# Kernel tuning notes

Hardware: AMD Instinct MI355X
Metric: run time of the kernel (lower is better)

Reference implementation:

```python
import jax, jax.numpy as jnp
import numpy as np

N_NODES = 100_000
N_RAND_EDGES = 1_600_000
NEG_SLOPE = 0.2


def setup_inputs() -> dict:
    key = jax.random.key(0)
    ks = jax.random.split(key, 12)
    inputs = jax.random.normal(ks[0], (N_NODES, 128), dtype=jnp.float32)
    # params (fc weight [in, H*D], attn vectors [H, D]); 0.1 scale for stability
    W0 = jax.random.normal(ks[1], (128, 4 * 32), dtype=jnp.float32) * 0.1
    al0 = jax.random.normal(ks[2], (4, 32), dtype=jnp.float32) * 0.1
    ar0 = jax.random.normal(ks[3], (4, 32), dtype=jnp.float32) * 0.1
    W1 = jax.random.normal(ks[4], (4 * 32, 4 * 32), dtype=jnp.float32) * 0.1
    al1 = jax.random.normal(ks[5], (4, 32), dtype=jnp.float32) * 0.1
    ar1 = jax.random.normal(ks[6], (4, 32), dtype=jnp.float32) * 0.1
    W2 = jax.random.normal(ks[7], (4 * 32, 1 * 40), dtype=jnp.float32) * 0.1
    al2 = jax.random.normal(ks[8], (1, 40), dtype=jnp.float32) * 0.1
    ar2 = jax.random.normal(ks[9], (1, 40), dtype=jnp.float32) * 0.1
    # edge list: random edges + self loops (guarantees in-degree >= 1)
    src = jnp.concatenate([
        jax.random.randint(ks[10], (N_RAND_EDGES,), 0, N_NODES, dtype=jnp.int32),
        jnp.arange(N_NODES, dtype=jnp.int32)])
    dst = jnp.concatenate([
        jax.random.randint(ks[11], (N_RAND_EDGES,), 0, N_NODES, dtype=jnp.int32),
        jnp.arange(N_NODES, dtype=jnp.int32)])
    return dict(inputs=inputs, W0=W0, al0=al0, ar0=ar0, W1=W1, al1=al1,
                ar1=ar1, W2=W2, al2=al2, ar2=ar2, src=src, dst=dst, empty=0)


def _gat_conv(h, W, al, ar, src, dst):
    """DGL-style GATConv (no dropout, no residual, no bias). Returns [N, H, D]."""
    N = h.shape[0]
    H, D = al.shape
    feat = (h @ W).reshape(N, H, D)
    el = jnp.sum(feat * al, axis=-1)  # [N, H]
    er = jnp.sum(feat * ar, axis=-1)  # [N, H]
    e = jax.nn.leaky_relu(el[src] + er[dst], negative_slope=NEG_SLOPE)  # [E, H]
    # edge softmax over incoming edges of each destination node (stable)
    m = jax.ops.segment_max(e, dst, num_segments=N)          # [N, H]
    ee = jnp.exp(e - m[dst])                                 # [E, H]
    denom = jax.ops.segment_sum(ee, dst, num_segments=N)     # [N, H]
    alpha = ee / denom[dst]                                  # [E, H]
    # gather source features, weight by attention, scatter-sum to destinations
    out = jax.ops.segment_sum(feat[src] * alpha[:, :, None], dst, num_segments=N)
    return out


def reference(inputs, W0, al0, ar0, W1, al1, ar1, W2, al2, ar2, src, dst, empty):
    N = inputs.shape[0]
    h = inputs
    for (W, al, ar) in ((W0, al0, ar0), (W1, al1, ar1)):
        h = jax.nn.elu(_gat_conv(h, W, al, ar, src, dst)).reshape(N, -1)
    logits = _gat_conv(h, W2, al2, ar2, src, dst).mean(axis=1)  # [N, num_classes]
    return jax.nn.log_softmax(logits, axis=1)
```

## Files before the change

kernel.cpp:

```cpp
#include <hip/hip_runtime.h>
#include <math.h>

typedef unsigned int uint32;
typedef unsigned short ushort;
typedef __attribute__((ext_vector_type(8))) short short8;
typedef __attribute__((ext_vector_type(4))) float f32x4;

__device__ inline uint32 bf16rn(float x){
  uint32 b = __float_as_uint(x);
  return (b + 0x7fffu + ((b>>16)&1u)) >> 16;
}
__device__ inline float bf16lo(uint32 v){ return __uint_as_float(v<<16); }
__device__ inline float bf16hi(uint32 v){ return __uint_as_float(v & 0xffff0000u); }

#define BKT_SHIFT 9
#define BKTCAP 12288
#define PCHUNK 4096
#define FB40S 64

__global__ __launch_bounds__(256) void k_partition(const int* __restrict__ src, const int* __restrict__ dst,
                        int* __restrict__ bkt_cursor, uint32* __restrict__ pairs, int E){
  __shared__ int cnt[512];
  __shared__ int base[512];
  int t = threadIdx.x;
  int blockBase = blockIdx.x * PCHUNK;
  for (int i=t; i<512; i+=256) cnt[i]=0;
  __syncthreads();
  #pragma unroll
  for (int i=0; i<PCHUNK/1024; i++){
    int e0 = blockBase + (i*256 + t)*4;
    if (e0+3 < E){
      int4 d4 = *(const int4*)&dst[e0];
      atomicAdd(&cnt[d4.x>>BKT_SHIFT],1);
      atomicAdd(&cnt[d4.y>>BKT_SHIFT],1);
      atomicAdd(&cnt[d4.z>>BKT_SHIFT],1);
      atomicAdd(&cnt[d4.w>>BKT_SHIFT],1);
    } else {
      for (int e=e0; e<E && e<e0+4; e++) atomicAdd(&cnt[dst[e]>>BKT_SHIFT],1);
    }
  }
  __syncthreads();
  for (int i=t; i<512; i+=256){
    int c = cnt[i];
    base[i] = c ? atomicAdd(&bkt_cursor[i], c) : 0;
    cnt[i] = 0;
  }
  __syncthreads();
  #pragma unroll
  for (int i=0; i<PCHUNK/1024; i++){
    int e0 = blockBase + (i*256 + t)*4;
    if (e0+3 < E){
      int4 s4 = *(const int4*)&src[e0];
      int4 d4 = *(const int4*)&dst[e0];
      int bx, pos;
      bx=d4.x>>BKT_SHIFT; pos=base[bx]+atomicAdd(&cnt[bx],1); if(pos<BKTCAP) pairs[(size_t)bx*BKTCAP+pos]=(uint32)s4.x|((uint32)(d4.x&511)<<22);
      bx=d4.y>>BKT_SHIFT; pos=base[bx]+atomicAdd(&cnt[bx],1); if(pos<BKTCAP) pairs[(size_t)bx*BKTCAP+pos]=(uint32)s4.y|((uint32)(d4.y&511)<<22);
      bx=d4.z>>BKT_SHIFT; pos=base[bx]+atomicAdd(&cnt[bx],1); if(pos<BKTCAP) pairs[(size_t)bx*BKTCAP+pos]=(uint32)s4.z|((uint32)(d4.z&511)<<22);
      bx=d4.w>>BKT_SHIFT; pos=base[bx]+atomicAdd(&cnt[bx],1); if(pos<BKTCAP) pairs[(size_t)bx*BKTCAP+pos]=(uint32)s4.w|((uint32)(d4.w&511)<<22);
    } else {
      for (int e=e0; e<E && e<e0+4; e++){
        int s=src[e], d=dst[e];
        int bx=d>>BKT_SHIFT; int pos=base[bx]+atomicAdd(&cnt[bx],1);
        if(pos<BKTCAP) pairs[(size_t)bx*BKTCAP+pos]=(uint32)s|((uint32)(d&511)<<22);
      }
    }
  }
}

__global__ __launch_bounds__(1024) void k_build(const int* __restrict__ bkt_cursor, int nb,
                        const uint32* __restrict__ pairs,
                        int* __restrict__ row_ptr, int* __restrict__ csr_src, int N){
  __shared__ int bscan[256];
  __shared__ int hist[512];
  __shared__ int sc[512];
  __shared__ int cur[512];
  int b = blockIdx.x;
  int t = threadIdx.x;
  int v0 = (t<256 && t<nb) ? min(bkt_cursor[t], BKTCAP) : 0;
  if (t<256) bscan[t] = v0;
  __syncthreads();
  int x0 = v0;
  for (int off=1; off<256; off<<=1){
    int y = (t<256 && t>=off) ? bscan[t-off] : 0;
    __syncthreads();
    if (t<256){ x0 += y; bscan[t] = x0; }
    __syncthreads();
  }
  int base = (b==0) ? 0 : bscan[b-1];
  if (b==0 && t==0) row_ptr[N] = bscan[nb-1];
  int cnt = bkt_cursor[b]; if (cnt > BKTCAP) cnt = BKTCAP;
  const uint32* p = pairs + (size_t)b*BKTCAP;
  if (t<512) hist[t]=0;
  __syncthreads();
  for (int i=t; i<cnt; i+=1024) atomicAdd(&hist[p[i]>>22], 1);
  __syncthreads();
  int v = (t<512)? hist[t] : 0;
  if (t<512) sc[t]=v;
  __syncthreads();
  int x=v;
  for (int off=1; off<512; off<<=1){
    int y = (t<512 && t>=off)? sc[t-off] : 0;
    __syncthreads();
    if (t<512){ x+=y; sc[t]=x; }
    __syncthreads();
  }
  if (t<512){
    int excl = x - v;
    int gnode = (b<<BKT_SHIFT) + t;
    if (gnode < N) row_ptr[gnode] = base + excl;
    cur[t] = excl;
  }
  __syncthreads();
  for (int i=t; i<cnt; i+=1024){
    uint32 e = p[i];
    int pos = atomicAdd(&cur[e>>22], 1);
    csr_src[base + pos] = (int)(e & 0x3FFFFFu);
  }
}

template<bool BF16A>
__global__ __launch_bounds__(256) void k_gemm128_mfma(const void* __restrict__ Av, const float* __restrict__ W,
                        const float* __restrict__ al, const float* __restrict__ ar,
                        ushort* __restrict__ Fb, float* __restrict__ el, float* __restrict__ er, int N){
  __shared__ __align__(16) ushort Wlds[128*128];
  __shared__ __align__(16) ushort Alds[64*128];
  __shared__ float sal[128], sar[128];
  int t = threadIdx.x;
  int rowBase = blockIdx.x*64;
  for (int i=t; i<8192; i+=256){
    int col = i & 127;
    int k2  = (i >> 7) * 2;
    float w0 = W[(size_t)k2*128 + col];
    float w1 = W[(size_t)(k2+1)*128 + col];
    uint32 pk = bf16rn(w0) | (bf16rn(w1)<<16);
    int byte = col*256 + k2*2;
    byte ^= (col&7)<<4;
    *(uint32*)((char*)Wlds + byte) = pk;
  }
  if (t < 128){ sal[t] = al[t]; sar[t] = ar[t]; }
  {
    int row = t>>2, k0 = (t&3)*32;
    int grow = rowBase + row;
    uint32 pk[16];
    if (grow < N){
      if constexpr (BF16A){
        const ushort* Ab = (const ushort*)Av;
        const uint4* ap = (const uint4*)(Ab + (size_t)grow*128 + k0);
        #pragma unroll
        for (int q=0;q<4;q++){ uint4 u = ap[q]; pk[q*4]=u.x; pk[q*4+1]=u.y; pk[q*4+2]=u.z; pk[q*4+3]=u.w; }
      } else {
        const float* Af = (const float*)Av;
        #pragma unroll
        for (int j=0;j<16;j++){
          float2 v = *(const float2*)(Af + (size_t)grow*128 + k0 + j*2);
          pk[j] = bf16rn(v.x) | (bf16rn(v.y)<<16);
        }
      }
    } else {
      #pragma unroll
      for (int j=0;j<16;j++) pk[j]=0u;
    }
    #pragma unroll
    for (int q=0;q<4;q++){
      int byte = row*256 + (k0 + q*8)*2;
      byte ^= (row&7)<<4;
      *(uint4*)((char*)Alds + byte) = make_uint4(pk[q*4],pk[q*4+1],pk[q*4+2],pk[q*4+3]);
    }
  }
  __syncthreads();
  int wid = t>>6, lane = t&63;
  int strip = wid*16;
  int lrow = lane & 15;
  int lk   = (lane>>4)*8;
  int swz  = (lrow&7)<<4;
  f32x4 acc[8];
  #pragma unroll
  for (int tc=0; tc<8; tc++) acc[tc] = (f32x4){0.f,0.f,0.f,0.f};
  #pragma unroll
  for (int kstep=0; kstep<4; kstep++){
    int kb = (kstep*32 + lk)*2;
    short8 bfrag = *(const short8*)((const char*)Alds + (((strip+lrow)*256 + kb) ^ swz));
    #pragma unroll
    for (int tc=0; tc<8; tc++){
      short8 afrag = *(const short8*)((const char*)Wlds + (((tc*16+lrow)*256 + kb) ^ swz));
      acc[tc] = __builtin_amdgcn_mfma_f32_16x16x32_bf16(afrag, bfrag, acc[tc], 0, 0, 0);
    }
  }
  int row = rowBase + strip + lrow;
  int cq = (lane>>4)*4;
  #pragma unroll
  for (int tc=0; tc<8; tc++){
    if (row < N){
      uint32 u0 = bf16rn(acc[tc][0]) | (bf16rn(acc[tc][1])<<16);
      uint32 u1 = bf16rn(acc[tc][2]) | (bf16rn(acc[tc][3])<<16);
      *(uint2*)(Fb + (size_t)row*128 + tc*16 + cq) = make_uint2(u0,u1);
    }
  }
  float hl[4] = {0.f,0.f,0.f,0.f};
  float hr[4] = {0.f,0.f,0.f,0.f};
  #pragma unroll
  for (int tc=0; tc<8; tc++){
    int cbase = tc*16 + cq;
    int h = tc>>1;
    #pragma unroll
    for (int r=0;r<4;r++){
      hl[h] = fmaf(acc[tc][r], sal[cbase+r], hl[h]);
      hr[h] = fmaf(acc[tc][r], sar[cbase+r], hr[h]);
    }
  }
  #pragma unroll
  for (int h=0;h<4;h++){
    hl[h] += __shfl_xor(hl[h],16); hl[h] += __shfl_xor(hl[h],32);
    hr[h] += __shfl_xor(hr[h],16); hr[h] += __shfl_xor(hr[h],32);
  }
  if (lane < 16 && row < N){
    *(float4*)&el[(size_t)row*4] = make_float4(hl[0],hl[1],hl[2],hl[3]);
    *(float4*)&er[(size_t)row*4] = make_float4(hr[0],hr[1],hr[2],hr[3]);
  }
}

__global__ __launch_bounds__(256) void k_agg128(const uint32* __restrict__ Fu, const float* __restrict__ el,
                         const float* __restrict__ er, const int* __restrict__ row_ptr,
                         const int* __restrict__ csr_src, ushort* __restrict__ out, int N){
  __shared__ float wlds[4][272];
  int t = threadIdx.x;
  int lane = t & 63;
  int wv = t >> 6;
  int node = (blockIdx.x*blockDim.x + t)>>6;
  if (__builtin_amdgcn_readfirstlane(node) >= N) return;
  int h = lane>>4;
  int i0 = lane & 15;
  float erv = er[(size_t)node*4+h];
  int beg = row_ptr[node], end = row_ptr[node+1];
  int ubeg = __builtin_amdgcn_readfirstlane(beg);
  int uend = __builtin_amdgcn_readfirstlane(end);
  int udeg = uend - ubeg;
  int sv = (lane < udeg) ? csr_src[ubeg+lane] : 0;
  int sn[4]; float evv[4];
  #pragma unroll
  for (int j=0;j<4;j++) sn[j] = __shfl(sv, i0 + 16*j);
  #pragma unroll
  for (int j=0;j<4;j++) evv[j] = el[(size_t)sn[j]*4+h];
  float w4[4];
  #pragma unroll
  for (int j=0;j<4;j++){
    float ev = evv[j] + erv;
    ev = ev>0.f ? ev : 0.2f*ev;
    w4[j] = (i0 + 16*j < udeg) ? __expf(ev) : 0.f;
  }
  float dsum = (w4[0]+w4[1]) + (w4[2]+w4[3]);
  dsum += __shfl_xor(dsum, 1);
  dsum += __shfl_xor(dsum, 2);
  dsum += __shfl_xor(dsum, 4);
  dsum += __shfl_xor(dsum, 8);
  int wb = h*68 + i0;
  wlds[wv][wb   ] = w4[0];
  wlds[wv][wb+16] = w4[1];
  wlds[wv][wb+32] = w4[2];
  wlds[wv][wb+48] = w4[3];
  const int* sp = csr_src + ubeg;
  const float* wp = &wlds[wv][h*68];
  float acc0=0.f, acc1=0.f;
  int nm = udeg > 64 ? 64 : udeg;
  uint32 vb[8];
  #pragma unroll
  for (int k=0;k<8;k++) vb[k] = (k<nm) ? Fu[(size_t)sp[k]*64 + lane] : 0u;
  int i=0;
  for (; i+16<=nm; i+=8){
    uint32 vn[8];
    #pragma unroll
    for (int k=0;k<8;k++) vn[k] = Fu[(size_t)sp[i+8+k]*64 + lane];
    #pragma unroll
    for (int k=0;k<8;k++){
      float wi = wp[i+k];
      acc0 = fmaf(wi, bf16lo(vb[k]), acc0);
      acc1 = fmaf(wi, bf16hi(vb[k]), acc1);
    }
    #pragma unroll
    for (int k=0;k<8;k++) vb[k]=vn[k];
  }
  {
    int lim = nm - i; if (lim > 8) lim = 8;
    #pragma unroll
    for (int k=0;k<8;k++) if (k<lim){
      float wi = wp[i+k];
      acc0 = fmaf(wi, bf16lo(vb[k]), acc0);
      acc1 = fmaf(wi, bf16hi(vb[k]), acc1);
    }
    for (int e=i+8; e<nm; e++){
      float wi = wp[e];
      uint32 v = Fu[(size_t)sp[e]*64 + lane];
      acc0 = fmaf(wi, bf16lo(v), acc0);
      acc1 = fmaf(wi, bf16hi(v), acc1);
    }
  }
  if (udeg > 64){
    for (int e=64; e<udeg; e++){
      int s = sp[e];
      float x = el[(size_t)s*4+h] + erv;
      x = x>0.f?x:0.2f*x; x=__expf(x);
      uint32 v = Fu[(size_t)s*64+lane];
      dsum += x;
      acc0 = fmaf(x, bf16lo(v), acc0);
      acc1 = fmaf(x, bf16hi(v), acc1);
    }
  }
  float inv = 1.0f/dsum;
  float o0 = acc0*inv, o1 = acc1*inv;
  o0 = o0>0.f ? o0 : expm1f(o0);
  o1 = o1>0.f ? o1 : expm1f(o1);
  uint32 uo = bf16rn(o0) | (bf16rn(o1)<<16);
  *(uint32*)(out + (size_t)node*128 + lane*2) = uo;
}

__global__ __launch_bounds__(256) void k_gemm42(const ushort* __restrict__ A, const float* __restrict__ W,
                        const float* __restrict__ al, const float* __restrict__ ar,
                        ushort* __restrict__ Fb, float* __restrict__ el, float* __restrict__ er, int N){
  __shared__ float wfull[128*48];
  __shared__ float hs[32][132];
  int t = threadIdx.x;
  int rowBase = blockIdx.x*128;
  for (int i=t; i<1280; i+=256){
    float4 v = *(const float4*)&W[i*4];
    int g = i*4;
    *(float4*)&wfull[(g/40)*48 + (g%40)] = v;
  }
  {
    int k = t & 127;
    const float* wrow = W + k*40;
    const float* a = (t < 128) ? al : ar;
    float s = 0.f;
    #pragma unroll
    for (int c=0;c<40;c++) s += wrow[c]*a[c];
    if (t < 128){
      wfull[k*48+40] = s;
      wfull[k*48+42] = 0.f; wfull[k*48+43] = 0.f; wfull[k*48+44] = 0.f;
    } else {
      wfull[k*48+41] = s;
      wfull[k*48+45] = 0.f; wfull[k*48+46] = 0.f; wfull[k*48+47] = 0.f;
    }
  }
  int c0 = (t&7)*6;
  int r0 = (t>>3)*4;
  float acc[4][6] = {};
  for (int kc=0; kc<128; kc+=32){
    {
      int row = t>>1; int kk0 = (t&1)*16;
      int grow = rowBase + row;
      if (grow < N){
        uint4 u0 = *(const uint4*)&A[(size_t)grow*128 + kc + kk0];
        uint4 u1 = *(const uint4*)&A[(size_t)grow*128 + kc + kk0 + 8];
        hs[kk0+ 0][row]=bf16lo(u0.x); hs[kk0+ 1][row]=bf16hi(u0.x);
        hs[kk0+ 2][row]=bf16lo(u0.y); hs[kk0+ 3][row]=bf16hi(u0.y);
        hs[kk0+ 4][row]=bf16lo(u0.z); hs[kk0+ 5][row]=bf16hi(u0.z);
        hs[kk0+ 6][row]=bf16lo(u0.w); hs[kk0+ 7][row]=bf16hi(u0.w);
        hs[kk0+ 8][row]=bf16lo(u1.x); hs[kk0+ 9][row]=bf16hi(u1.x);
        hs[kk0+10][row]=bf16lo(u1.y); hs[kk0+11][row]=bf16hi(u1.y);
        hs[kk0+12][row]=bf16lo(u1.z); hs[kk0+13][row]=bf16hi(u1.z);
        hs[kk0+14][row]=bf16lo(u1.w); hs[kk0+15][row]=bf16hi(u1.w);
      } else {
        #pragma unroll
        for (int j=0;j<16;j++) hs[kk0+j][row]=0.f;
      }
    }
    __syncthreads();
    #pragma unroll
    for (int k=0;k<32;k++){
      float4 av = *(const float4*)&hs[k][r0];
      const float* wp = &wfull[(kc+k)*48 + c0];
      float2 b01 = *(const float2*)&wp[0];
      float2 b23 = *(const float2*)&wp[2];
      float2 b45 = *(const float2*)&wp[4];
      float a4[4] = {av.x,av.y,av.z,av.w};
      float b6[6] = {b01.x,b01.y,b23.x,b23.y,b45.x,b45.y};
      #pragma unroll
      for (int r=0;r<4;r++)
        #pragma unroll
        for (int c=0;c<6;c++)
          acc[r][c] = fmaf(a4[r], b6[c], acc[r][c]);
    }
    __syncthreads();
  }
  #pragma unroll
  for (int r=0;r<4;r++){
    int row = rowBase + r0 + r;
    if (row >= N) break;
    if (c0 < 40){
      #pragma unroll
      for (int j=0;j<6;j+=2){
        int col = c0 + j;
        if (col < 40){
          uint32 u = bf16rn(acc[r][j]) | (bf16rn(acc[r][j+1])<<16);
          *(uint32*)(Fb + (size_t)row*FB40S + col) = u;
        }
      }
      if (c0 == 36){ el[row] = acc[r][4]; er[row] = acc[r][5]; }
    }
  }
}

__global__ __launch_bounds__(256) void k_agg40(const ushort* __restrict__ Fb, const float* __restrict__ el,
                       const float* __restrict__ er, const int* __restrict__ row_ptr,
                       const int* __restrict__ csr_src, float* __restrict__ out, int N){
  __shared__ float wlds[4][64];
  int t = threadIdx.x;
  int lane = t & 63;
  int wv = t >> 6;
  int node = (blockIdx.x*blockDim.x + t)>>6;
  if (__builtin_amdgcn_readfirstlane(node) >= N) return;
  bool act = lane<40;
  int l40 = act ? lane : 0;
  float erv = er[node];
  int beg = row_ptr[node], end = row_ptr[node+1];
  int ubeg = __builtin_amdgcn_readfirstlane(beg);
  int uend = __builtin_amdgcn_readfirstlane(end);
  int udeg = uend - ubeg;
  int sv = (lane < udeg) ? csr_src[ubeg+lane] : 0;
  float w = 0.f;
  if (lane < udeg){
    float ev = el[sv] + erv;
    ev = ev>0.f ? ev : 0.2f*ev;
    w = __expf(ev);
  }
  float dsum = w;
  dsum += __shfl_xor(dsum, 1);
  dsum += __shfl_xor(dsum, 2);
  dsum += __shfl_xor(dsum, 4);
  dsum += __shfl_xor(dsum, 8);
  dsum += __shfl_xor(dsum, 16);
  dsum += __shfl_xor(dsum, 32);
  wlds[wv][lane] = w;
  const int* sp = csr_src + ubeg;
  float acc=0.f;
  int nm = udeg > 64 ? 64 : udeg;
  ushort fb8[8];
  #pragma unroll
  for (int k=0;k<8;k++) fb8[k] = (k<nm) ? Fb[(size_t)sp[k]*FB40S + l40] : (ushort)0;
  int i=0;
  for (; i+16<=nm; i+=8){
    ushort fn[8];
    #pragma unroll
    for (int k=0;k<8;k++) fn[k] = Fb[(size_t)sp[i+8+k]*FB40S + l40];
    #pragma unroll
    for (int k=0;k<8;k++){
      float wi = wlds[wv][i+k];
      acc = fmaf(wi, __uint_as_float(((uint32)fb8[k])<<16), acc);
    }
    #pragma unroll
    for (int k=0;k<8;k++) fb8[k]=fn[k];
  }
  {
    int lim = nm - i; if (lim > 8) lim = 8;
    #pragma unroll
    for (int k=0;k<8;k++) if (k<lim){
      float wi = wlds[wv][i+k];
      acc = fmaf(wi, __uint_as_float(((uint32)fb8[k])<<16), acc);
    }
    for (int e=i+8; e<nm; e++){
      float wi = wlds[wv][e];
      ushort f = Fb[(size_t)sp[e]*FB40S + l40];
      acc = fmaf(wi, __uint_as_float(((uint32)f)<<16), acc);
    }
  }
  if (udeg > 64){
    for (int e=64; e<udeg; e++){
      int s = sp[e];
      float x = el[s] + erv;
      x = x>0.f?x:0.2f*x; x=__expf(x);
      ushort f = Fb[(size_t)s*FB40S + l40];
      dsum += x;
      acc = fmaf(x, __uint_as_float(((uint32)f)<<16), acc);
    }
  }
  float logit = acc/dsum;
  float m = act ? logit : -INFINITY;
  for (int off=32; off; off>>=1) m = fmaxf(m, __shfl_xor(m, off));
  float ex = act ? expf(logit - m) : 0.f;
  float ssum = ex;
  for (int off=32; off; off>>=1) ssum += __shfl_xor(ssum, off);
  if (act) out[(size_t)node*40 + lane] = logit - m - logf(ssum);
}

extern "C" void kernel_launch(void* const* d_in, const int* in_sizes, int n_in,
                              void* d_out, int out_size, void* d_ws, size_t ws_size,
                              hipStream_t stream){
  const float* inputs = (const float*)d_in[0];
  const float* W0  = (const float*)d_in[1];
  const float* al0 = (const float*)d_in[2];
  const float* ar0 = (const float*)d_in[3];
  const float* W1  = (const float*)d_in[4];
  const float* al1 = (const float*)d_in[5];
  const float* ar1 = (const float*)d_in[6];
  const float* W2  = (const float*)d_in[7];
  const float* al2 = (const float*)d_in[8];
  const float* ar2 = (const float*)d_in[9];
  const int* src = (const int*)d_in[10];
  const int* dst = (const int*)d_in[11];
  int N = in_sizes[0]/128;
  int E = in_sizes[10];
  int NB = (N + (1<<BKT_SHIFT) - 1) >> BKT_SHIFT;

  char* p = (char*)d_ws;
  auto carve = [&](size_t bytes)->char*{ char* q=p; p += ((bytes+255)/256)*256; return q; };
  ushort* Fb   = (ushort*)carve((size_t)N*128*2);
  ushort* Fb40 = (ushort*)carve((size_t)N*FB40S*2);
  ushort* bufH = (ushort*)carve((size_t)N*128*2);
  float* el  = (float*)carve((size_t)N*4*4);
  float* er  = (float*)carve((size_t)N*4*4);
  float* el2 = (float*)carve((size_t)N*4);
  float* er2 = (float*)carve((size_t)N*4);
  int* bkt_cursor  = (int*)carve((size_t)NB*4);
  int* row_ptr = (int*)carve((size_t)(N+1)*4);
  int* csr_src = (int*)carve((size_t)E*4);

  uint32* pairs = (uint32*)bufH;

  hipMemsetAsync(bkt_cursor, 0, (size_t)NB*4, stream);
  int nPB = (E + PCHUNK - 1) / PCHUNK;
  k_partition<<<nPB, 256, 0, stream>>>(src, dst, bkt_cursor, pairs, E);
  k_build    <<<NB, 1024, 0, stream>>>(bkt_cursor, NB, pairs, row_ptr, csr_src, N);

  int gRows = (N+63)/64;
  int gWave = (N+3)/4;
  int gRows42 = (N+127)/128;
  k_gemm128_mfma<false><<<gRows,256,0,stream>>>(inputs, W0, al0, ar0, Fb, el, er, N);
  k_agg128 <<<gWave,256,0,stream>>>((const uint32*)Fb, el, er, row_ptr, csr_src, bufH, N);
  k_gemm128_mfma<true><<<gRows,256,0,stream>>>(bufH, W1, al1, ar1, Fb, el, er, N);
  k_agg128 <<<gWave,256,0,stream>>>((const uint32*)Fb, el, er, row_ptr, csr_src, bufH, N);
  k_gemm42 <<<gRows42,256,0,stream>>>(bufH, W2, al2, ar2, Fb40, el2, er2, N);
  k_agg40  <<<gWave,256,0,stream>>>(Fb40, el2, er2, row_ptr, csr_src, (float*)d_out, N);
}
```

Baseline: 347.7 us.

## Merge edge partition and first-layer GEMM into one heterogeneous launch

```diff
diff --git a/kernel.cpp b/kernel.cpp
--- a/kernel.cpp
+++ b/kernel.cpp
@@ -18,52 +18,144 @@
 #define PCHUNK 4096
 #define FB40S 64
 
-__global__ __launch_bounds__(256) void k_partition(const int* __restrict__ src, const int* __restrict__ dst,
-                        int* __restrict__ bkt_cursor, uint32* __restrict__ pairs, int E){
-  __shared__ int cnt[512];
-  __shared__ int base[512];
+__global__ __launch_bounds__(256) void k_part_gemm0(const int* __restrict__ src, const int* __restrict__ dst,
+                        int* __restrict__ bkt_cursor, uint32* __restrict__ pairs, int E, int nPB,
+                        const float* __restrict__ A, const float* __restrict__ W,
+                        const float* __restrict__ al, const float* __restrict__ ar,
+                        ushort* __restrict__ Fb, float* __restrict__ el, float* __restrict__ er, int N){
+  __shared__ __align__(16) ushort Wlds[128*128];
+  __shared__ __align__(16) ushort Alds[64*128];
+  __shared__ float sal[128], sar[128];
   int t = threadIdx.x;
-  int blockBase = blockIdx.x * PCHUNK;
-  for (int i=t; i<512; i+=256) cnt[i]=0;
+  if (blockIdx.x < nPB){
+    int* cnt  = (int*)Wlds;
+    int* base = ((int*)Wlds) + 512;
+    int blockBase = blockIdx.x * PCHUNK;
+    for (int i=t; i<512; i+=256) cnt[i]=0;
+    __syncthreads();
+    #pragma unroll
+    for (int i=0; i<PCHUNK/1024; i++){
+      int e0 = blockBase + (i*256 + t)*4;
+      if (e0+3 < E){
+        int4 d4 = *(const int4*)&dst[e0];
+        atomicAdd(&cnt[d4.x>>BKT_SHIFT],1);
+        atomicAdd(&cnt[d4.y>>BKT_SHIFT],1);
+        atomicAdd(&cnt[d4.z>>BKT_SHIFT],1);
+        atomicAdd(&cnt[d4.w>>BKT_SHIFT],1);
+      } else {
+        for (int e=e0; e<E && e<e0+4; e++) atomicAdd(&cnt[dst[e]>>BKT_SHIFT],1);
+      }
+    }
+    __syncthreads();
+    for (int i=t; i<512; i+=256){
+      int c = cnt[i];
+      base[i] = c ? atomicAdd(&bkt_cursor[i], c) : 0;
+      cnt[i] = 0;
+    }
+    __syncthreads();
+    #pragma unroll
+    for (int i=0; i<PCHUNK/1024; i++){
+      int e0 = blockBase + (i*256 + t)*4;
+      if (e0+3 < E){
+        int4 s4 = *(const int4*)&src[e0];
+        int4 d4 = *(const int4*)&dst[e0];
+        int bx, pos;
+        bx=d4.x>>BKT_SHIFT; pos=base[bx]+atomicAdd(&cnt[bx],1); if(pos<BKTCAP) pairs[(size_t)bx*BKTCAP+pos]=(uint32)s4.x|((uint32)(d4.x&511)<<22);
+        bx=d4.y>>BKT_SHIFT; pos=base[bx]+atomicAdd(&cnt[bx],1); if(pos<BKTCAP) pairs[(size_t)bx*BKTCAP+pos]=(uint32)s4.y|((uint32)(d4.y&511)<<22);
+        bx=d4.z>>BKT_SHIFT; pos=base[bx]+atomicAdd(&cnt[bx],1); if(pos<BKTCAP) pairs[(size_t)bx*BKTCAP+pos]=(uint32)s4.z|((uint32)(d4.z&511)<<22);
+        bx=d4.w>>BKT_SHIFT; pos=base[bx]+atomicAdd(&cnt[bx],1); if(pos<BKTCAP) pairs[(size_t)bx*BKTCAP+pos]=(uint32)s4.w|((uint32)(d4.w&511)<<22);
+      } else {
+        for (int e=e0; e<E && e<e0+4; e++){
+          int s=src[e], d=dst[e];
+          int bx=d>>BKT_SHIFT; int pos=base[bx]+atomicAdd(&cnt[bx],1);
+          if(pos<BKTCAP) pairs[(size_t)bx*BKTCAP+pos]=(uint32)s|((uint32)(d&511)<<22);
+        }
+      }
+    }
+    return;
+  }
+  int rowBase = (blockIdx.x - nPB)*64;
+  for (int i=t; i<8192; i+=256){
+    int col = i & 127;
+    int k2  = (i >> 7) * 2;
+    float w0 = W[(size_t)k2*128 + col];
+    float w1 = W[(size_t)(k2+1)*128 + col];
+    uint32 pk = bf16rn(w0) | (bf16rn(w1)<<16);
+    int byte = col*256 + k2*2;
+    byte ^= (col&7)<<4;
+    *(uint32*)((char*)Wlds + byte) = pk;
+  }
+  if (t < 128){ sal[t] = al[t]; sar[t] = ar[t]; }
+  {
+    int row = t>>2, k0 = (t&3)*32;
+    int grow = rowBase + row;
+    uint32 pk[16];
+    if (grow < N){
+      #pragma unroll
+      for (int j=0;j<16;j++){
+        float2 v = *(const float2*)(A + (size_t)grow*128 + k0 + j*2);
+        pk[j] = bf16rn(v.x) | (bf16rn(v.y)<<16);
+      }
+    } else {
+      #pragma unroll
+      for (int j=0;j<16;j++) pk[j]=0u;
+    }
+    #pragma unroll
+    for (int q=0;q<4;q++){
+      int byte = row*256 + (k0 + q*8)*2;
+      byte ^= (row&7)<<4;
+      *(uint4*)((char*)Alds + byte) = make_uint4(pk[q*4],pk[q*4+1],pk[q*4+2],pk[q*4+3]);
+    }
+  }
   __syncthreads();
-  #pragma unroll
-  for (int i=0; i<PCHUNK/1024; i++){
-    int e0 = blockBase + (i*256 + t)*4;
-    if (e0+3 < E){
-      int4 d4 = *(const int4*)&dst[e0];
-      atomicAdd(&cnt[d4.x>>BKT_SHIFT],1);
-      atomicAdd(&cnt[d4.y>>BKT_SHIFT],1);
-      atomicAdd(&cnt[d4.z>>BKT_SHIFT],1);
-      atomicAdd(&cnt[d4.w>>BKT_SHIFT],1);
-    } else {
-      for (int e=e0; e<E && e<e0+4; e++) atomicAdd(&cnt[dst[e]>>BKT_SHIFT],1);
-    }
-  }
-  __syncthreads();
-  for (int i=t; i<512; i+=256){
-    int c = cnt[i];
-    base[i] = c ? atomicAdd(&bkt_cursor[i], c) : 0;
-    cnt[i] = 0;
-  }
-  __syncthreads();
-  #pragma unroll
-  for (int i=0; i<PCHUNK/1024; i++){
-    int e0 = blockBase + (i*256 + t)*4;
-    if (e0+3 < E){
-      int4 s4 = *(const int4*)&src[e0];
-      int4 d4 = *(const int4*)&dst[e0];
-      int bx, pos;
-      bx=d4.x>>BKT_SHIFT; pos=base[bx]+atomicAdd(&cnt[bx],1); if(pos<BKTCAP) pairs[(size_t)bx*BKTCAP+pos]=(uint32)s4.x|((uint32)(d4.x&511)<<22);
-      bx=d4.y>>BKT_SHIFT; pos=base[bx]+atomicAdd(&cnt[bx],1); if(pos<BKTCAP) pairs[(size_t)bx*BKTCAP+pos]=(uint32)s4.y|((uint32)(d4.y&511)<<22);
-      bx=d4.z>>BKT_SHIFT; pos=base[bx]+atomicAdd(&cnt[bx],1); if(pos<BKTCAP) pairs[(size_t)bx*BKTCAP+pos]=(uint32)s4.z|((uint32)(d4.z&511)<<22);
-      bx=d4.w>>BKT_SHIFT; pos=base[bx]+atomicAdd(&cnt[bx],1); if(pos<BKTCAP) pairs[(size_t)bx*BKTCAP+pos]=(uint32)s4.w|((uint32)(d4.w&511)<<22);
-    } else {
-      for (int e=e0; e<E && e<e0+4; e++){
-        int s=src[e], d=dst[e];
-        int bx=d>>BKT_SHIFT; int pos=base[bx]+atomicAdd(&cnt[bx],1);
-        if(pos<BKTCAP) pairs[(size_t)bx*BKTCAP+pos]=(uint32)s|((uint32)(d&511)<<22);
-      }
-    }
+  int wid = t>>6, lane = t&63;
+  int strip = wid*16;
+  int lrow = lane & 15;
+  int lk   = (lane>>4)*8;
+  int swz  = (lrow&7)<<4;
+  f32x4 acc[8];
+  #pragma unroll
+  for (int tc=0; tc<8; tc++) acc[tc] = (f32x4){0.f,0.f,0.f,0.f};
+  #pragma unroll
+  for (int kstep=0; kstep<4; kstep++){
+    int kb = (kstep*32 + lk)*2;
+    short8 bfrag = *(const short8*)((const char*)Alds + (((strip+lrow)*256 + kb) ^ swz));
+    #pragma unroll
+    for (int tc=0; tc<8; tc++){
+      short8 afrag = *(const short8*)((const char*)Wlds + (((tc*16+lrow)*256 + kb) ^ swz));
+      acc[tc] = __builtin_amdgcn_mfma_f32_16x16x32_bf16(afrag, bfrag, acc[tc], 0, 0, 0);
+    }
+  }
+  int row = rowBase + strip + lrow;
+  int cq = (lane>>4)*4;
+  #pragma unroll
+  for (int tc=0; tc<8; tc++){
+    if (row < N){
+      uint32 u0 = bf16rn(acc[tc][0]) | (bf16rn(acc[tc][1])<<16);
+      uint32 u1 = bf16rn(acc[tc][2]) | (bf16rn(acc[tc][3])<<16);
+      *(uint2*)(Fb + (size_t)row*128 + tc*16 + cq) = make_uint2(u0,u1);
+    }
+  }
+  float hl[4] = {0.f,0.f,0.f,0.f};
+  float hr[4] = {0.f,0.f,0.f,0.f};
+  #pragma unroll
+  for (int tc=0; tc<8; tc++){
+    int cbase = tc*16 + cq;
+    int h = tc>>1;
+    #pragma unroll
+    for (int r=0;r<4;r++){
+      hl[h] = fmaf(acc[tc][r], sal[cbase+r], hl[h]);
+      hr[h] = fmaf(acc[tc][r], sar[cbase+r], hr[h]);
+    }
+  }
+  #pragma unroll
+  for (int h=0;h<4;h++){
+    hl[h] += __shfl_xor(hl[h],16); hl[h] += __shfl_xor(hl[h],32);
+    hr[h] += __shfl_xor(hr[h],16); hr[h] += __shfl_xor(hr[h],32);
+  }
+  if (lane < 16 && row < N){
+    *(float4*)&el[(size_t)row*4] = make_float4(hl[0],hl[1],hl[2],hl[3]);
+    *(float4*)&er[(size_t)row*4] = make_float4(hr[0],hr[1],hr[2],hr[3]);
   }
 }
 
@@ -118,8 +210,7 @@
   }
 }
 
-template<bool BF16A>
-__global__ __launch_bounds__(256) void k_gemm128_mfma(const void* __restrict__ Av, const float* __restrict__ W,
+__global__ __launch_bounds__(256) void k_gemm128_mfma(const ushort* __restrict__ Ab, const float* __restrict__ W,
                         const float* __restrict__ al, const float* __restrict__ ar,
                         ushort* __restrict__ Fb, float* __restrict__ el, float* __restrict__ er, int N){
   __shared__ __align__(16) ushort Wlds[128*128];
@@ -143,19 +234,9 @@
     int grow = rowBase + row;
     uint32 pk[16];
     if (grow < N){
-      if constexpr (BF16A){
-        const ushort* Ab = (const ushort*)Av;
-        const uint4* ap = (const uint4*)(Ab + (size_t)grow*128 + k0);
-        #pragma unroll
-        for (int q=0;q<4;q++){ uint4 u = ap[q]; pk[q*4]=u.x; pk[q*4+1]=u.y; pk[q*4+2]=u.z; pk[q*4+3]=u.w; }
-      } else {
-        const float* Af = (const float*)Av;
-        #pragma unroll
-        for (int j=0;j<16;j++){
-          float2 v = *(const float2*)(Af + (size_t)grow*128 + k0 + j*2);
-          pk[j] = bf16rn(v.x) | (bf16rn(v.y)<<16);
-        }
-      }
+      const uint4* ap = (const uint4*)(Ab + (size_t)grow*128 + k0);
+      #pragma unroll
+      for (int q=0;q<4;q++){ uint4 u = ap[q]; pk[q*4]=u.x; pk[q*4+1]=u.y; pk[q*4+2]=u.z; pk[q*4+3]=u.w; }
     } else {
       #pragma unroll
       for (int j=0;j<16;j++) pk[j]=0u;
@@ -517,15 +598,15 @@
 
   hipMemsetAsync(bkt_cursor, 0, (size_t)NB*4, stream);
   int nPB = (E + PCHUNK - 1) / PCHUNK;
-  k_partition<<<nPB, 256, 0, stream>>>(src, dst, bkt_cursor, pairs, E);
-  k_build    <<<NB, 1024, 0, stream>>>(bkt_cursor, NB, pairs, row_ptr, csr_src, N);
-
   int gRows = (N+63)/64;
   int gWave = (N+3)/4;
   int gRows42 = (N+127)/128;
-  k_gemm128_mfma<false><<<gRows,256,0,stream>>>(inputs, W0, al0, ar0, Fb, el, er, N);
+
+  k_part_gemm0<<<nPB+gRows, 256, 0, stream>>>(src, dst, bkt_cursor, pairs, E, nPB,
+                                              inputs, W0, al0, ar0, Fb, el, er, N);
+  k_build <<<NB, 1024, 0, stream>>>(bkt_cursor, NB, pairs, row_ptr, csr_src, N);
   k_agg128 <<<gWave,256,0,stream>>>((const uint32*)Fb, el, er, row_ptr, csr_src, bufH, N);
-  k_gemm128_mfma<true><<<gRows,256,0,stream>>>(bufH, W1, al1, ar1, Fb, el, er, N);
+  k_gemm128_mfma<<<gRows,256,0,stream>>>(bufH, W1, al1, ar1, Fb, el, er, N);
   k_agg128 <<<gWave,256,0,stream>>>((const uint32*)Fb, el, er, row_ptr, csr_src, bufH, N);
   k_gemm42 <<<gRows42,256,0,stream>>>(bufH, W2, al2, ar2, Fb40, el2, er2, N);
   k_agg40  <<<gWave,256,0,stream>>>(Fb40, el2, er2, row_ptr, csr_src, (float*)d_out, N);
```

New measurement: 340.6 us. 2.1% less time.
